# Kernel tuning notes

Hardware: AMD Instinct MI355X
Metric: run time of the kernel (lower is better)

The kernel has to match this reference:

```python
import jax, jax.numpy as jnp
import numpy as np

HIDDEN = 128
STATE = 64
ACTION = 16
D_IO = STATE + ACTION  # 80
BATCH = 4096
SEQ_LEN = 512


def setup_inputs() -> dict:
    key = jax.random.key(0)
    ks = jax.random.split(key, 7)
    s = 1.0 / np.sqrt(HIDDEN)
    return {
        "quantized_hn": jax.random.normal(ks[0], (BATCH, HIDDEN), jnp.float32),
        "W_ih": jax.random.uniform(ks[1], (4 * HIDDEN, D_IO), jnp.float32, -s, s),
        "W_hh": jax.random.uniform(ks[2], (4 * HIDDEN, HIDDEN), jnp.float32, -s, s),
        "b_ih": jax.random.uniform(ks[3], (4 * HIDDEN,), jnp.float32, -s, s),
        "b_hh": jax.random.uniform(ks[4], (4 * HIDDEN,), jnp.float32, -s, s),
        "W_fc": jax.random.uniform(ks[5], (D_IO, HIDDEN), jnp.float32, -s, s),
        "b_fc": jax.random.uniform(ks[6], (D_IO,), jnp.float32, -s, s),
        "seq_len": SEQ_LEN,
    }


def reference(quantized_hn, W_ih, W_hh, b_ih, b_hh, W_fc, b_fc, seq_len):
    B, H = quantized_hn.shape
    D = W_fc.shape[0]

    def step(carry, _):
        h, c, x = carry  # h,c: (B,H); x: (B,D)
        # PyTorch LSTM gate order: i, f, g, o
        gates = x @ W_ih.T + b_ih + h @ W_hh.T + b_hh  # (B, 4H)
        i, f, g, o = jnp.split(gates, 4, axis=-1)
        c_new = jax.nn.sigmoid(f) * c + jax.nn.sigmoid(i) * jnp.tanh(g)
        h_new = jax.nn.sigmoid(o) * jnp.tanh(c_new)
        y = h_new @ W_fc.T + b_fc  # (B, D) -> fed back as next input
        return (h_new, c_new, y), y

    h0 = quantized_hn
    c0 = jnp.zeros((B, H), quantized_hn.dtype)
    x0 = jnp.zeros((B, D), quantized_hn.dtype)
    _, ys = jax.lax.scan(step, (h0, c0, x0), None, length=seq_len)
    return jnp.transpose(ys, (1, 0, 2))  # (B, seq_len, D)
```

## Files before the change

kernel.cpp:

```cpp
#include <hip/hip_runtime.h>

typedef __bf16 bf16_t;
typedef __bf16 bf16x8 __attribute__((ext_vector_type(8)));
typedef float  f32x4  __attribute__((ext_vector_type(4)));

#define HID    128
#define DIO    80
#define G4     512
#define TSTEP  512
#define BB     16
#define NBATCH 4096
#define NBLK   (NBATCH / BB)
#define HSTR   136

__device__ bf16_t g_weff_frags[128 * 512];
__device__ bf16_t g_whh_frags[128 * 512];
__device__ bf16_t g_wfc_frags[20 * 512];
__device__ float  g_weff[G4 * HID];
__device__ float  g_beff[G4];
__device__ float  g_b1[G4];

__global__ void k_weff(const float* __restrict__ W_ih, const float* __restrict__ W_hh,
                       const float* __restrict__ b_ih, const float* __restrict__ b_hh,
                       const float* __restrict__ W_fc, const float* __restrict__ b_fc) {
  int gid = blockIdx.x * blockDim.x + threadIdx.x;
  int g = gid >> 7, k = gid & 127;
  float acc = W_hh[g * HID + k];
#pragma unroll 8
  for (int d = 0; d < DIO; ++d)
    acc = fmaf(W_ih[g * DIO + d], W_fc[d * HID + k], acc);
  g_weff[g * HID + k] = acc;
  if (k == 0) {
    float bb = b_ih[g] + b_hh[g];
    g_b1[g] = bb;
    float be = bb;
    for (int d = 0; d < DIO; ++d) be = fmaf(W_ih[g * DIO + d], b_fc[d], be);
    g_beff[g] = be;
  }
}

__global__ void k_frag(const float* __restrict__ W_hh, const float* __restrict__ W_fc) {
  int tile = blockIdx.x;
  int lane = threadIdx.x;
  int c = lane & 15, q = lane >> 4;
  if (tile < 128) {
    int gtile = tile >> 2, kt = tile & 3;
    int n = gtile * 16 + c;
#pragma unroll
    for (int j = 0; j < 8; ++j)
      g_weff_frags[tile * 512 + lane * 8 + j] = (bf16_t)g_weff[n * HID + kt * 32 + q * 8 + j];
  } else if (tile < 256) {
    int t2 = tile - 128;
    int gtile = t2 >> 2, kt = t2 & 3;
    int n = gtile * 16 + c;
#pragma unroll
    for (int j = 0; j < 8; ++j)
      g_whh_frags[t2 * 512 + lane * 8 + j] = (bf16_t)W_hh[n * HID + kt * 32 + q * 8 + j];
  } else {
    int t2 = tile - 256;
    int yt = t2 >> 2, kt = t2 & 3;
    int n = yt * 16 + c;
#pragma unroll
    for (int j = 0; j < 8; ++j)
      g_wfc_frags[t2 * 512 + lane * 8 + j] = (bf16_t)W_fc[n * HID + kt * 32 + q * 8 + j];
  }
}

__device__ __forceinline__ float fsigm(float x) {
  return __builtin_amdgcn_rcpf(1.0f + __builtin_amdgcn_exp2f(x * -1.4426950408889634f));
}
__device__ __forceinline__ float ftanh(float x) {
  return 1.0f - 2.0f * __builtin_amdgcn_rcpf(1.0f + __builtin_amdgcn_exp2f(x * 2.8853900817779268f));
}

__global__ __launch_bounds__(256, 1) void k_lstm(const float* __restrict__ h0,
                                                 const float* __restrict__ b_fc,
                                                 float* __restrict__ out) {
  __shared__ __align__(16) bf16_t hbuf[2][BB * HSTR];
  const int tid = threadIdx.x;
  const int lane = tid & 63;
  const int w = tid >> 6;
  const int c = lane & 15, q = lane >> 4;
  const int b0 = blockIdx.x * BB;

  for (int i = tid; i < BB * HID; i += 256) {
    int r = i >> 7, k = i & 127;
    hbuf[0][r * HSTR + k] = (bf16_t)h0[(long)(b0 + r) * HID + k];
  }

  bf16x8 Wy[2][4];
  f32x4  ybias[2];
  {
    float by = b_fc[w * 16 + c];
    ybias[0] = (f32x4){by, by, by, by};
#pragma unroll
    for (int kt = 0; kt < 4; ++kt)
      Wy[0][kt] = *(const bf16x8*)&g_wfc_frags[(w * 4 + kt) * 512 + lane * 8];
  }
  if (w == 0) {
    float by = b_fc[64 + c];
    ybias[1] = (f32x4){by, by, by, by};
#pragma unroll
    for (int kt = 0; kt < 4; ++kt)
      Wy[1][kt] = *(const bf16x8*)&g_wfc_frags[(16 + kt) * 512 + lane * 8];
  }

  bf16x8 Wg[4][2][4];
  float  bias[4][2];
  auto load_wg = [&](const bf16_t* frags, const float* bsrc) {
#pragma unroll
    for (int G = 0; G < 4; ++G)
#pragma unroll
      for (int s = 0; s < 2; ++s) {
        int gtile = G * 8 + w * 2 + s;
        bias[G][s] = bsrc[gtile * 16 + c];
#pragma unroll
        for (int kt = 0; kt < 4; ++kt)
          Wg[G][s][kt] = *(const bf16x8*)&frags[(gtile * 4 + kt) * 512 + lane * 8];
      }
  };

  f32x4 cst[2] = {(f32x4){0, 0, 0, 0}, (f32x4){0, 0, 0, 0}};
  bf16x8 hf[4];

  __syncthreads();
#pragma unroll
  for (int kt = 0; kt < 4; ++kt)
    hf[kt] = *(const bf16x8*)&hbuf[0][c * HSTR + kt * 32 + q * 8];

  float* outp = out + (long)(b0 + q * 4) * TSTEP * DIO + w * 16 + c;

  auto step = [&](int t) {
    f32x4 acc[4][2];
#pragma unroll
    for (int G = 0; G < 4; ++G)
#pragma unroll
      for (int s = 0; s < 2; ++s)
        acc[G][s] = (f32x4){bias[G][s], bias[G][s], bias[G][s], bias[G][s]};
#pragma unroll
    for (int kt = 0; kt < 4; ++kt)
#pragma unroll
      for (int G = 0; G < 4; ++G)
#pragma unroll
        for (int s = 0; s < 2; ++s)
          acc[G][s] = __builtin_amdgcn_mfma_f32_16x16x32_bf16(hf[kt], Wg[G][s][kt], acc[G][s], 0, 0, 0);
    const int buf = t & 1;
#pragma unroll
    for (int s = 0; s < 2; ++s)
#pragma unroll
      for (int r = 0; r < 4; ++r) {
        float iv = fsigm(acc[0][s][r]);
        float fv = fsigm(acc[1][s][r]);
        float gv = ftanh(acc[2][s][r]);
        float ov = fsigm(acc[3][s][r]);
        float cn = fv * cst[s][r] + iv * gv;
        cst[s][r] = cn;
        hbuf[buf][(q * 4 + r) * HSTR + w * 32 + s * 16 + c] = (bf16_t)(ov * ftanh(cn));
      }
    __syncthreads();
#pragma unroll
    for (int kt = 0; kt < 4; ++kt)
      hf[kt] = *(const bf16x8*)&hbuf[buf][c * HSTR + kt * 32 + q * 8];
    f32x4 ya = ybias[0];
#pragma unroll
    for (int kt = 0; kt < 4; ++kt)
      ya = __builtin_amdgcn_mfma_f32_16x16x32_bf16(hf[kt], Wy[0][kt], ya, 0, 0, 0);
#pragma unroll
    for (int r = 0; r < 4; ++r)
      outp[(long)r * TSTEP * DIO + (long)(t - 1) * DIO] = ya[r];
    if (w == 0) {
      f32x4 yb = ybias[1];
#pragma unroll
      for (int kt = 0; kt < 4; ++kt)
        yb = __builtin_amdgcn_mfma_f32_16x16x32_bf16(hf[kt], Wy[1][kt], yb, 0, 0, 0);
#pragma unroll
      for (int r = 0; r < 4; ++r)
        outp[(long)r * TSTEP * DIO + (long)(t - 1) * DIO + 64] = yb[r];
    }
  };

  load_wg(g_whh_frags, g_b1);
  step(1);
  load_wg(g_weff_frags, g_beff);
  for (int t = 2; t <= TSTEP; ++t) step(t);
}

extern "C" void kernel_launch(void* const* d_in, const int* in_sizes, int n_in,
                              void* d_out, int out_size, void* d_ws, size_t ws_size,
                              hipStream_t stream) {
  const float* h0   = (const float*)d_in[0];
  const float* W_ih = (const float*)d_in[1];
  const float* W_hh = (const float*)d_in[2];
  const float* b_ih = (const float*)d_in[3];
  const float* b_hh = (const float*)d_in[4];
  const float* W_fc = (const float*)d_in[5];
  const float* b_fc = (const float*)d_in[6];
  float* out = (float*)d_out;

  k_weff<<<256, 256, 0, stream>>>(W_ih, W_hh, b_ih, b_hh, W_fc, b_fc);
  k_frag<<<276, 64, 0, stream>>>(W_hh, W_fc);
  k_lstm<<<NBLK, 256, 0, stream>>>(h0, b_fc, out);
}
```

Measured before the change: 1.136 ms.

## Use 8 waves per block with transposed MFMA operands and vectorized stores

Doubles the block to 512 threads (8 waves), so each wave owns one 16-column tile per gate instead of two. Swapping the MFMA operands makes each lane hold four consecutive hidden units for one batch row, which allows packed bf16x4 writes to LDS and f32x4 vector stores to the output. The output projection is spread across 5 waves instead of 4 plus one extra on wave 0. This halves per-wave weight registers so two blocks can share a CU, at the cost of more waves joining each per-step barrier.

```diff
diff --git a/kernel.cpp b/kernel.cpp
--- a/kernel.cpp
+++ b/kernel.cpp
@@ -1,6 +1,7 @@
 #include <hip/hip_runtime.h>
 
 typedef __bf16 bf16_t;
+typedef __bf16 bf16x4 __attribute__((ext_vector_type(4)));
 typedef __bf16 bf16x8 __attribute__((ext_vector_type(8)));
 typedef float  f32x4  __attribute__((ext_vector_type(4)));
 
@@ -73,7 +74,7 @@
   return 1.0f - 2.0f * __builtin_amdgcn_rcpf(1.0f + __builtin_amdgcn_exp2f(x * 2.8853900817779268f));
 }
 
-__global__ __launch_bounds__(256, 1) void k_lstm(const float* __restrict__ h0,
+__global__ __launch_bounds__(512, 2) void k_lstm(const float* __restrict__ h0,
                                                  const float* __restrict__ b_fc,
                                                  float* __restrict__ out) {
   __shared__ __align__(16) bf16_t hbuf[2][BB * HSTR];
@@ -83,44 +84,36 @@
   const int c = lane & 15, q = lane >> 4;
   const int b0 = blockIdx.x * BB;
 
-  for (int i = tid; i < BB * HID; i += 256) {
+  for (int i = tid; i < BB * HID; i += 512) {
     int r = i >> 7, k = i & 127;
     hbuf[0][r * HSTR + k] = (bf16_t)h0[(long)(b0 + r) * HID + k];
   }
 
-  bf16x8 Wy[2][4];
-  f32x4  ybias[2];
-  {
-    float by = b_fc[w * 16 + c];
-    ybias[0] = (f32x4){by, by, by, by};
+  bf16x8 Wy[4];
+  f32x4  ybias;
+  if (w < 5) {
 #pragma unroll
     for (int kt = 0; kt < 4; ++kt)
-      Wy[0][kt] = *(const bf16x8*)&g_wfc_frags[(w * 4 + kt) * 512 + lane * 8];
-  }
-  if (w == 0) {
-    float by = b_fc[64 + c];
-    ybias[1] = (f32x4){by, by, by, by};
+      Wy[kt] = *(const bf16x8*)&g_wfc_frags[(w * 4 + kt) * 512 + lane * 8];
 #pragma unroll
-    for (int kt = 0; kt < 4; ++kt)
-      Wy[1][kt] = *(const bf16x8*)&g_wfc_frags[(16 + kt) * 512 + lane * 8];
+    for (int r = 0; r < 4; ++r) ybias[r] = b_fc[w * 16 + q * 4 + r];
   }
 
-  bf16x8 Wg[4][2][4];
-  float  bias[4][2];
+  bf16x8 Wg[4][4];
+  f32x4  bias[4];
   auto load_wg = [&](const bf16_t* frags, const float* bsrc) {
 #pragma unroll
-    for (int G = 0; G < 4; ++G)
+    for (int G = 0; G < 4; ++G) {
+      int gtile = G * 8 + w;
 #pragma unroll
-      for (int s = 0; s < 2; ++s) {
-        int gtile = G * 8 + w * 2 + s;
-        bias[G][s] = bsrc[gtile * 16 + c];
+      for (int r = 0; r < 4; ++r) bias[G][r] = bsrc[gtile * 16 + q * 4 + r];
 #pragma unroll
-        for (int kt = 0; kt < 4; ++kt)
-          Wg[G][s][kt] = *(const bf16x8*)&frags[(gtile * 4 + kt) * 512 + lane * 8];
-      }
+      for (int kt = 0; kt < 4; ++kt)
+        Wg[G][kt] = *(const bf16x8*)&frags[(gtile * 4 + kt) * 512 + lane * 8];
+    }
   };
 
-  f32x4 cst[2] = {(f32x4){0, 0, 0, 0}, (f32x4){0, 0, 0, 0}};
+  f32x4 cst = (f32x4){0, 0, 0, 0};
   bf16x8 hf[4];
 
   __syncthreads();
@@ -128,54 +121,42 @@
   for (int kt = 0; kt < 4; ++kt)
     hf[kt] = *(const bf16x8*)&hbuf[0][c * HSTR + kt * 32 + q * 8];
 
-  float* outp = out + (long)(b0 + q * 4) * TSTEP * DIO + w * 16 + c;
+  float* outp = out + (long)(b0 + c) * TSTEP * DIO + w * 16 + q * 4;
 
   auto step = [&](int t) {
-    f32x4 acc[4][2];
+    f32x4 acc[4];
 #pragma unroll
-    for (int G = 0; G < 4; ++G)
-#pragma unroll
-      for (int s = 0; s < 2; ++s)
-        acc[G][s] = (f32x4){bias[G][s], bias[G][s], bias[G][s], bias[G][s]};
+    for (int G = 0; G < 4; ++G) acc[G] = bias[G];
 #pragma unroll
     for (int kt = 0; kt < 4; ++kt)
 #pragma unroll
       for (int G = 0; G < 4; ++G)
+        acc[G] = __builtin_amdgcn_mfma_f32_16x16x32_bf16(Wg[G][kt], hf[kt], acc[G], 0, 0, 0);
+
+    const int buf = t & 1;
+    bf16x4 hv;
 #pragma unroll
-        for (int s = 0; s < 2; ++s)
-          acc[G][s] = __builtin_amdgcn_mfma_f32_16x16x32_bf16(hf[kt], Wg[G][s][kt], acc[G][s], 0, 0, 0);
-    const int buf = t & 1;
-#pragma unroll
-    for (int s = 0; s < 2; ++s)
-#pragma unroll
-      for (int r = 0; r < 4; ++r) {
-        float iv = fsigm(acc[0][s][r]);
-        float fv = fsigm(acc[1][s][r]);
-        float gv = ftanh(acc[2][s][r]);
-        float ov = fsigm(acc[3][s][r]);
-        float cn = fv * cst[s][r] + iv * gv;
-        cst[s][r] = cn;
-        hbuf[buf][(q * 4 + r) * HSTR + w * 32 + s * 16 + c] = (bf16_t)(ov * ftanh(cn));
-      }
+    for (int r = 0; r < 4; ++r) {
+      float iv = fsigm(acc[0][r]);
+      float fv = fsigm(acc[1][r]);
+      float gv = ftanh(acc[2][r]);
+      float ov = fsigm(acc[3][r]);
+      float cn = fv * cst[r] + iv * gv;
+      cst[r] = cn;
+      hv[r] = (bf16_t)(ov * ftanh(cn));
+    }
+    *(bf16x4*)&hbuf[buf][c * HSTR + w * 16 + q * 4] = hv;
     __syncthreads();
 #pragma unroll
     for (int kt = 0; kt < 4; ++kt)
       hf[kt] = *(const bf16x8*)&hbuf[buf][c * HSTR + kt * 32 + q * 8];
-    f32x4 ya = ybias[0];
-#pragma unroll
-    for (int kt = 0; kt < 4; ++kt)
-      ya = __builtin_amdgcn_mfma_f32_16x16x32_bf16(hf[kt], Wy[0][kt], ya, 0, 0, 0);
-#pragma unroll
-    for (int r = 0; r < 4; ++r)
-      outp[(long)r * TSTEP * DIO + (long)(t - 1) * DIO] = ya[r];
-    if (w == 0) {
-      f32x4 yb = ybias[1];
+
+    if (w < 5) {
+      f32x4 ya = ybias;
 #pragma unroll
       for (int kt = 0; kt < 4; ++kt)
-        yb = __builtin_amdgcn_mfma_f32_16x16x32_bf16(hf[kt], Wy[1][kt], yb, 0, 0, 0);
-#pragma unroll
-      for (int r = 0; r < 4; ++r)
-        outp[(long)r * TSTEP * DIO + (long)(t - 1) * DIO + 64] = yb[r];
+        ya = __builtin_amdgcn_mfma_f32_16x16x32_bf16(Wy[kt], hf[kt], ya, 0, 0, 0);
+      *(f32x4*)&outp[(long)(t - 1) * DIO] = ya;
     }
   };
 
@@ -199,5 +180,5 @@
 
   k_weff<<<256, 256, 0, stream>>>(W_ih, W_hh, b_ih, b_hh, W_fc, b_fc);
   k_frag<<<276, 64, 0, stream>>>(W_hh, W_fc);
-  k_lstm<<<NBLK, 256, 0, stream>>>(h0, b_fc, out);
+  k_lstm<<<NBLK, 512, 0, stream>>>(h0, b_fc, out);
 }
```

After: 1.004 ms. -11.6%, faster.
